# Optimization experiments

Measured on AMD Instinct MI355X. Metric: run time of the kernel, lower is better.

The kernel has to match this reference:

```python
import jax, jax.numpy as jnp
import numpy as np

B, S, R = 1, 128, 384          # batch, n_seq (MSA rows), n_res
C_M, C_Z, H, D = 256, 128, 8, 32  # msa channels, pair channels, heads, head dim


def layernorm(x, g, b, eps=1e-5):
    mu = jnp.mean(x, axis=-1, keepdims=True)
    var = jnp.var(x, axis=-1, keepdims=True)
    return (x - mu) * jax.lax.rsqrt(var + eps) * g + b


def setup_inputs() -> dict:
    key = jax.random.key(0)
    ks = jax.random.split(key, 10)
    w = lambda k, shape: jax.random.normal(k, shape, jnp.float32) * 0.02
    return {
        "msa_act": jax.random.normal(ks[0], (B, S, R, C_M), jnp.float32),
        "pair_act": jax.random.normal(ks[1], (B, R, R, C_Z), jnp.float32),
        "msa_mask": jnp.ones((B, S, R), jnp.float32),
        "qn_g": jnp.ones((C_M,), jnp.float32),
        "qn_b": jnp.zeros((C_M,), jnp.float32),
        "pn_g": jnp.ones((C_Z,), jnp.float32),
        "pn_b": jnp.zeros((C_Z,), jnp.float32),
        "w_pair": w(ks[2], (C_Z, H)),           # feat_2d_weights (no bias)
        "wq": w(ks[3], (C_M, H, D)),
        "wk": w(ks[4], (C_M, H, D)),
        "wv": w(ks[5], (C_M, H, D)),
        "wg": w(ks[6], (C_M, H, D)),            # gating linear
        "bg": jnp.ones((H, D), jnp.float32),     # gating bias (AF2 inits to 1)
        "wo": w(ks[7], (H, D, C_M)),             # output projection
        "bo": jnp.zeros((C_M,), jnp.float32),
    }


def reference(msa_act, pair_act, msa_mask, qn_g, qn_b, pn_g, pn_b,
              w_pair, wq, wk, wv, wg, bg, wo, bo):
    # pair bias: LN + Linear(c_z -> H), -> [B, 1, H, R, R]
    z = jnp.einsum('bijc,ch->bhij', layernorm(pair_act, pn_g, pn_b), w_pair)[:, None]
    # mask bias: [B, S, 1, 1, R]
    mask_bias = (1e9 * (msa_mask - 1.0))[:, :, None, None, :]

    m = layernorm(msa_act, qn_g, qn_b)
    q = jnp.einsum('bsrc,chd->bshrd', m, wq) * (D ** -0.5)
    k = jnp.einsum('bsrc,chd->bshrd', m, wk)
    v = jnp.einsum('bsrc,chd->bshrd', m, wv)

    logits = jnp.einsum('bshqd,bshkd->bshqk', q, k) + mask_bias + z  # [B,S,H,R,R]
    a = jax.nn.softmax(logits, axis=-1)
    o = jnp.einsum('bshqk,bshkd->bsqhd', a, v)                       # [B,S,R,H,D]

    g = jax.nn.sigmoid(jnp.einsum('bsrc,chd->bsrhd', m, wg) + bg)
    out = jnp.einsum('bsrhd,hdc->bsrc', o * g, wo) + bo              # [B,S,R,C_M]
    return out
```

## Files before the change

### kernel.cpp

```cpp
#include <hip/hip_runtime.h>
#include <hip/hip_bf16.h>

typedef unsigned int uint;
typedef unsigned short ushortT;
typedef __attribute__((ext_vector_type(8))) short bf16x8;
typedef __attribute__((ext_vector_type(4))) float f32x4;

#define S_ 128
#define R_ 384
#define CM 256
#define CZ 128
#define H_ 8
#define D_ 32
#define SR (S_*R_)
#define RRTOT (R_*R_)
#define SHRD (S_*H_*R_*D_)

__device__ __forceinline__ float bf2f(ushortT u) {
    return __uint_as_float(((uint)u) << 16);
}
__device__ __forceinline__ ushortT f2bf(float f) {
    uint x = __float_as_uint(f);
    x += 0x7FFFu + ((x >> 16) & 1u);
    return (ushortT)(x >> 16);
}
__device__ __forceinline__ uint pack_bf2(float lo, float hi) {
    return (uint)f2bf(lo) | ((uint)f2bf(hi) << 16);
}

__global__ __launch_bounds__(256) void k_prep(
        const float* __restrict__ wq, const float* __restrict__ wk,
        const float* __restrict__ wv, const float* __restrict__ wg,
        const float* __restrict__ wo,
        ushortT* __restrict__ wt, ushortT* __restrict__ wgt,
        ushortT* __restrict__ wot) {
    int id = blockIdx.x * 256 + threadIdx.x;
    int which = id >> 16, r16 = id & 65535;
    int y = r16 & 255, x = r16 >> 8;
    if (which == 0)      wt[(size_t)y*256 + x]       = f2bf(wq[(size_t)x*256 + y] * 0.17677669529663687f);
    else if (which == 1) wt[(size_t)(256+y)*256 + x] = f2bf(wk[(size_t)x*256 + y]);
    else if (which == 2) wt[(size_t)(512+y)*256 + x] = f2bf(wv[(size_t)x*256 + y]);
    else if (which == 3) wgt[(size_t)y*256 + x]      = f2bf(wg[(size_t)x*256 + y]);
    else                 wot[(size_t)y*256 + x]      = f2bf(wo[(size_t)x*256 + y]);
}

__global__ __launch_bounds__(256) void k_pair_bias(
        const float* __restrict__ pair, const float* __restrict__ pn_g,
        const float* __restrict__ pn_b, const float* __restrict__ w_pair,
        ushortT* __restrict__ z) {
    int wave = threadIdx.x >> 6, lane = threadIdx.x & 63;
    int row = blockIdx.x * 4 + wave;
    const float* x = pair + (size_t)row * CZ;
    float2 xv = *(const float2*)&x[lane * 2];
    float s  = xv.x + xv.y;
    float s2 = xv.x*xv.x + xv.y*xv.y;
    #pragma unroll
    for (int off = 32; off; off >>= 1) {
        s  += __shfl_xor(s,  off);
        s2 += __shfl_xor(s2, off);
    }
    float mu  = s * (1.0f / 128.0f);
    float var = s2 * (1.0f / 128.0f) - mu * mu;
    float rstd = rsqrtf(var + 1e-5f);
    float2 gv = *(const float2*)&pn_g[lane * 2];
    float2 bv = *(const float2*)&pn_b[lane * 2];
    float n0 = (xv.x - mu) * rstd * gv.x + bv.x;
    float n1 = (xv.y - mu) * rstd * gv.y + bv.y;
    float4 wa = *(const float4*)&w_pair[lane*16     ];
    float4 wb = *(const float4*)&w_pair[lane*16 +  4];
    float4 wc = *(const float4*)&w_pair[lane*16 +  8];
    float4 wd = *(const float4*)&w_pair[lane*16 + 12];
    float v0_ = n0*wa.x + n1*wc.x, v1_ = n0*wa.y + n1*wc.y;
    float v2_ = n0*wa.z + n1*wc.z, v3_ = n0*wa.w + n1*wc.w;
    float v4_ = n0*wb.x + n1*wd.x, v5_ = n0*wb.y + n1*wd.y;
    float v6_ = n0*wb.z + n1*wd.z, v7_ = n0*wb.w + n1*wd.w;
    float x0 = __shfl_xor(v0_,1), x1 = __shfl_xor(v1_,1), x2 = __shfl_xor(v2_,1), x3 = __shfl_xor(v3_,1);
    float x4 = __shfl_xor(v4_,1), x5 = __shfl_xor(v5_,1), x6 = __shfl_xor(v6_,1), x7 = __shfl_xor(v7_,1);
    bool b0 = (lane & 1) != 0;
    float u0 = b0 ? v4_+x4 : v0_+x0;
    float u1 = b0 ? v5_+x5 : v1_+x1;
    float u2 = b0 ? v6_+x6 : v2_+x2;
    float u3 = b0 ? v7_+x7 : v3_+x3;
    float y0 = __shfl_xor(u0,2), y1 = __shfl_xor(u1,2), y2 = __shfl_xor(u2,2), y3 = __shfl_xor(u3,2);
    bool b1 = (lane & 2) != 0;
    float w0 = b1 ? u2+y2 : u0+y0;
    float w1 = b1 ? u3+y3 : u1+y1;
    float z0 = __shfl_xor(w0,4), z1 = __shfl_xor(w1,4);
    bool b2 = (lane & 4) != 0;
    float val = b2 ? w1+z1 : w0+z0;
    val += __shfl_xor(val, 8);
    val += __shfl_xor(val, 16);
    val += __shfl_xor(val, 32);
    int hmap = 4*(lane & 1) + 2*((lane >> 1) & 1) + ((lane >> 2) & 1);
    if (lane < 8) z[(size_t)hmap * RRTOT + row] = f2bf(val);
}

__device__ __forceinline__ void ln_row_f4(
        const float* __restrict__ src, const float* __restrict__ gam,
        const float* __restrict__ bet, char* msb, int row, int lane) {
    float4 xv = *(const float4*)&src[lane * 4];
    float sm = (xv.x + xv.y) + (xv.z + xv.w);
    float s2 = (xv.x*xv.x + xv.y*xv.y) + (xv.z*xv.z + xv.w*xv.w);
    #pragma unroll
    for (int off = 32; off; off >>= 1) {
        sm += __shfl_xor(sm, off);
        s2 += __shfl_xor(s2, off);
    }
    float mu  = sm * (1.0f / 256.0f);
    float var = s2 * (1.0f / 256.0f) - mu * mu;
    float rstd = rsqrtf(var + 1e-5f);
    float4 gv = *(const float4*)&gam[lane * 4];
    float4 bv = *(const float4*)&bet[lane * 4];
    float n0 = (xv.x - mu) * rstd * gv.x + bv.x, n1 = (xv.y - mu) * rstd * gv.y + bv.y;
    float n2 = (xv.z - mu) * rstd * gv.z + bv.z, n3 = (xv.w - mu) * rstd * gv.w + bv.w;
    uint2 w; w.x = pack_bf2(n0, n1); w.y = pack_bf2(n2, n3);
    *(uint2*)(msb + ((row*512 + lane*8) ^ ((row & 7) << 4))) = w;
}

__global__ __launch_bounds__(256) void k_msa_qkv(
        const float* __restrict__ msa, const float* __restrict__ qn_g,
        const float* __restrict__ qn_b, const ushortT* __restrict__ wt,
        ushortT* __restrict__ qo, ushortT* __restrict__ ko,
        ushortT* __restrict__ vto) {
    __shared__ ushortT m_sh[32 * 256];
    __shared__ ushortT o_sh[32 * 256];
    int tid = threadIdx.x, wave = tid >> 6, lane = tid & 63;
    int c = lane & 15, g = (lane >> 4) & 3;
    int r0 = blockIdx.x * 32, s = r0 / R_, rl0 = r0 % R_;
    char* msb = (char*)m_sh;
    char* osb = (char*)o_sh;

    #pragma unroll
    for (int i = 0; i < 8; ++i) {
        int row = wave * 8 + i;
        ln_row_f4(msa + (size_t)(r0 + row) * CM, qn_g, qn_b, msb, row, lane);
    }
    __syncthreads();

    bf16x8 af[2][8];
    #pragma unroll
    for (int rt = 0; rt < 2; ++rt)
        #pragma unroll
        for (int kc = 0; kc < 8; ++kc) {
            int row = rt*16 + c;
            af[rt][kc] = *(const bf16x8*)(msb + ((row*512 + (kc*32 + 8*g)*2) ^ ((c & 7) << 4)));
        }

    const f32x4 z4 = {0.f, 0.f, 0.f, 0.f};
    for (int mI = 0; mI < 3; ++mI) {
        int tb = wave * 4;
        const ushortT* wb0 = wt + ((size_t)(mI*256 + tb*16 + c)) * 256 + 8*g;
        const ushortT* wb1 = wb0 + 16*256;
        const ushortT* wb2 = wb0 + 32*256;
        const ushortT* wb3 = wb0 + 48*256;
        f32x4 a0L = z4, a0H = z4, a1L = z4, a1H = z4;
        f32x4 a2L = z4, a2H = z4, a3L = z4, a3H = z4;
        #pragma unroll
        for (int kc = 0; kc < 8; ++kc) {
            bf16x8 b0 = *(const bf16x8*)(wb0 + kc*32);
            bf16x8 b1 = *(const bf16x8*)(wb1 + kc*32);
            bf16x8 b2 = *(const bf16x8*)(wb2 + kc*32);
            bf16x8 b3 = *(const bf16x8*)(wb3 + kc*32);
            a0L = __builtin_amdgcn_mfma_f32_16x16x32_bf16(af[0][kc], b0, a0L, 0, 0, 0);
            a0H = __builtin_amdgcn_mfma_f32_16x16x32_bf16(af[1][kc], b0, a0H, 0, 0, 0);
            a1L = __builtin_amdgcn_mfma_f32_16x16x32_bf16(af[0][kc], b1, a1L, 0, 0, 0);
            a1H = __builtin_amdgcn_mfma_f32_16x16x32_bf16(af[1][kc], b1, a1H, 0, 0, 0);
            a2L = __builtin_amdgcn_mfma_f32_16x16x32_bf16(af[0][kc], b2, a2L, 0, 0, 0);
            a2H = __builtin_amdgcn_mfma_f32_16x16x32_bf16(af[1][kc], b2, a2H, 0, 0, 0);
            a3L = __builtin_amdgcn_mfma_f32_16x16x32_bf16(af[0][kc], b3, a3L, 0, 0, 0);
            a3H = __builtin_amdgcn_mfma_f32_16x16x32_bf16(af[1][kc], b3, a3H, 0, 0, 0);
        }
        #pragma unroll
        for (int j = 0; j < 4; ++j) {
            f32x4 lo = (j == 0) ? a0L : (j == 1) ? a1L : (j == 2) ? a2L : a3L;
            f32x4 hi = (j == 0) ? a0H : (j == 1) ? a1H : (j == 2) ? a2H : a3H;
            if (mI < 2) {
                int col = (tb + j)*16 + c;
                #pragma unroll
                for (int r = 0; r < 4; ++r) {
                    int row0 = 4*g + r, row1 = row0 + 16;
                    *(ushortT*)(osb + ((row0*512 + col*2) ^ ((row0 & 7) << 4))) = f2bf(lo[r]);
                    *(ushortT*)(osb + ((row1*512 + col*2) ^ ((row1 & 7) << 4))) = f2bf(hi[r]);
                }
            } else {
                int hd = (tb + j)*16 + c;
                #pragma unroll
                for (int r = 0; r < 4; ++r) {
                    int rlo = 4*g + r, rhi = rlo + 16;
                    *(ushortT*)(osb + ((hd*64 + rlo*2) ^ ((hd & 3) << 4))) = f2bf(lo[r]);
                    *(ushortT*)(osb + ((hd*64 + rhi*2) ^ ((hd & 3) << 4))) = f2bf(hi[r]);
                }
            }
        }
        __syncthreads();
        if (mI < 2) {
            ushortT* O = (mI == 0) ? qo : ko;
            #pragma unroll
            for (int i = 0; i < 4; ++i) {
                int idx = tid + i*256;
                int row = idx >> 5, c16 = idx & 31;
                uint4 vd = *(const uint4*)(osb + ((row*512 + c16*16) ^ ((row & 7) << 4)));
                int hh = c16 >> 2, dq = (c16 & 3) * 8;
                size_t ga = ((size_t)(s*H_ + hh) * R_ + rl0 + row) * D_ + dq;
                *(uint4*)&O[ga] = vd;
            }
        } else {
            #pragma unroll
            for (int i = 0; i < 4; ++i) {
                int idx = tid + i*256;
                int hd = idx >> 2, q8 = idx & 3;
                uint4 vd = *(const uint4*)(osb + ((hd*64 + q8*16) ^ ((hd & 3) << 4)));
                size_t ga = ((size_t)(s*256 + hd)) * R_ + rl0 + q8*8;
                *(uint4*)&vto[ga] = vd;
            }
        }
        __syncthreads();
    }
}

__global__ __launch_bounds__(512) void k_attn(
        const ushortT* __restrict__ qws, const ushortT* __restrict__ kws,
        const ushortT* __restrict__ vtws, const ushortT* __restrict__ zws,
        const float* __restrict__ mask, float* __restrict__ out) {
    __shared__ ushortT k_sh[R_ * 40];
    __shared__ ushortT vt_sh[D_ * R_];
    __shared__ float   mb[R_];
    __shared__ ushortT p_sh[8 * 1280];
    int tid = threadIdx.x, wave = tid >> 6, lane = tid & 63;
    int c = lane & 15, g = (lane >> 4) & 3;
    int s = blockIdx.x >> 3, h = blockIdx.x & 7;
    size_t base = (size_t)(s * H_ + h) * R_ * D_;

    {
        const uint4* ks = (const uint4*)(kws + base);
        char* kb_ = (char*)k_sh;
        for (int i = tid; i < 1536; i += 512) {
            int row = i >> 2, part = i & 3;
            *(uint4*)(kb_ + row*80 + part*16) = ks[i];
        }
        const uint4* vs = (const uint4*)(vtws + base);
        char* vb = (char*)vt_sh;
        for (int i = tid; i < 1536; i += 512) {
            int d = i / 48, ch = i % 48;
            *(uint4*)(vb + ((d*768 + ch*16) ^ ((d & 7) << 4))) = vs[i];
        }
        for (int j = tid; j < R_; j += 512) mb[j] = 1e9f * (mask[s*R_ + j] - 1.0f);
    }
    __syncthreads();

    const char* ksb = (const char*)k_sh;
    const char* vtb = (const char*)vt_sh;
    char* psb = (char*)p_sh + wave * 2560;
    const f32x4 zero4 = {0.f, 0.f, 0.f, 0.f};

    for (int qt = wave; qt < 24; qt += 8) {
        int q0 = qt * 16;
        bf16x8 qf = *(const bf16x8*)(qws + base + (size_t)(q0 + c) * D_ + 8*g);
        const ushortT* zq = zws + (size_t)h * RRTOT + (size_t)(q0 + c) * R_ + 4*g;

        float sm = 0.f;
        f32x4 o0 = zero4, o1 = zero4;
        #pragma unroll 2
        for (int kb = 0; kb < 12; ++kb) {
            bf16x8 kfA = *(const bf16x8*)(ksb + ((2*kb    )*16 + c)*80 + 16*g);
            bf16x8 kfB = *(const bf16x8*)(ksb + ((2*kb + 1)*16 + c)*80 + 16*g);
            f32x4 pA = __builtin_amdgcn_mfma_f32_16x16x32_bf16(kfA, qf, zero4, 0, 0, 0);
            f32x4 pB = __builtin_amdgcn_mfma_f32_16x16x32_bf16(kfB, qf, zero4, 0, 0, 0);
            float4 mvA = *(const float4*)&mb[(2*kb    )*16 + 4*g];
            float4 mvB = *(const float4*)&mb[(2*kb + 1)*16 + 4*g];
            ushort4 zvA = *(const ushort4*)(zq + (2*kb    )*16);
            ushort4 zvB = *(const ushort4*)(zq + (2*kb + 1)*16);
            pA.x = __expf(pA.x + mvA.x + bf2f(zvA.x));
            pA.y = __expf(pA.y + mvA.y + bf2f(zvA.y));
            pA.z = __expf(pA.z + mvA.z + bf2f(zvA.z));
            pA.w = __expf(pA.w + mvA.w + bf2f(zvA.w));
            pB.x = __expf(pB.x + mvB.x + bf2f(zvB.x));
            pB.y = __expf(pB.y + mvB.y + bf2f(zvB.y));
            pB.z = __expf(pB.z + mvB.z + bf2f(zvB.z));
            pB.w = __expf(pB.w + mvB.w + bf2f(zvB.w));
            sm += (pA.x + pA.y) + (pA.z + pA.w) + (pB.x + pB.y) + (pB.z + pB.w);
            uint2 wA; wA.x = pack_bf2(pA.x, pA.y); wA.y = pack_bf2(pA.z, pA.w);
            uint2 wB; wB.x = pack_bf2(pB.x, pB.y); wB.y = pack_bf2(pB.z, pB.w);
            *(uint2*)(psb + (kb&1)*1280 + c*80 +      8*g) = wA;
            *(uint2*)(psb + (kb&1)*1280 + c*80 + 32 + 8*g) = wB;
            bf16x8 pa = *(const bf16x8*)(psb + (kb&1)*1280 + c*80 + 16*g);
            bf16x8 v0 = *(const bf16x8*)(vtb + (((c     )*768 + kb*64 + 16*g) ^ ((c & 7) << 4)));
            bf16x8 v1 = *(const bf16x8*)(vtb + (((16 + c)*768 + kb*64 + 16*g) ^ ((c & 7) << 4)));
            o0 = __builtin_amdgcn_mfma_f32_16x16x32_bf16(v0, pa, o0, 0, 0, 0);
            o1 = __builtin_amdgcn_mfma_f32_16x16x32_bf16(v1, pa, o1, 0, 0, 0);
        }
        sm += __shfl_xor(sm, 16);
        sm += __shfl_xor(sm, 32);
        float inv = 1.0f / sm;
        float4 s0, s1;
        s0.x = o0[0]*inv; s0.y = o0[1]*inv; s0.z = o0[2]*inv; s0.w = o0[3]*inv;
        s1.x = o1[0]*inv; s1.y = o1[1]*inv; s1.z = o1[2]*inv; s1.w = o1[3]*inv;
        float* ob = out + (size_t)(s*R_ + q0 + c) * CM + h*D_ + 4*g;
        *(float4*)ob = s0;
        *(float4*)(ob + 16) = s1;
    }
}

__global__ __launch_bounds__(256) void k_out(
        const float* __restrict__ msa, const float* __restrict__ qn_g,
        const float* __restrict__ qn_b, const ushortT* __restrict__ wgt,
        const float* __restrict__ bg, const ushortT* __restrict__ wot,
        const float* __restrict__ bo, float* __restrict__ out) {
    __shared__ ushortT m_sh[32 * 256];
    __shared__ ushortT og_sh[32 * 256];
    int tid = threadIdx.x, wave = tid >> 6, lane = tid & 63;
    int c = lane & 15, g = (lane >> 4) & 3;
    int r0 = blockIdx.x * 32;
    char* msb = (char*)m_sh;
    char* ogb = (char*)og_sh;

    #pragma unroll
    for (int i = 0; i < 8; ++i) {
        int row = wave * 8 + i;
        ln_row_f4(msa + (size_t)(r0 + row) * CM, qn_g, qn_b, msb, row, lane);
    }
    __syncthreads();

    bf16x8 af[2][8];
    #pragma unroll
    for (int rt = 0; rt < 2; ++rt)
        #pragma unroll
        for (int kc = 0; kc < 8; ++kc) {
            int row = rt*16 + c;
            af[rt][kc] = *(const bf16x8*)(msb + ((row*512 + (kc*32 + 8*g)*2) ^ ((c & 7) << 4)));
        }

    const f32x4 z4 = {0.f, 0.f, 0.f, 0.f};
    {
        int tb = wave * 4;
        const ushortT* wb0 = wgt + (size_t)(tb*16 + c) * 256 + 8*g;
        const ushortT* wb1 = wb0 + 16*256;
        const ushortT* wb2 = wb0 + 32*256;
        const ushortT* wb3 = wb0 + 48*256;
        f32x4 a0L = z4, a0H = z4, a1L = z4, a1H = z4;
        f32x4 a2L = z4, a2H = z4, a3L = z4, a3H = z4;
        #pragma unroll
        for (int kc = 0; kc < 8; ++kc) {
            bf16x8 b0 = *(const bf16x8*)(wb0 + kc*32);
            bf16x8 b1 = *(const bf16x8*)(wb1 + kc*32);
            bf16x8 b2 = *(const bf16x8*)(wb2 + kc*32);
            bf16x8 b3 = *(const bf16x8*)(wb3 + kc*32);
            a0L = __builtin_amdgcn_mfma_f32_16x16x32_bf16(af[0][kc], b0, a0L, 0, 0, 0);
            a0H = __builtin_amdgcn_mfma_f32_16x16x32_bf16(af[1][kc], b0, a0H, 0, 0, 0);
            a1L = __builtin_amdgcn_mfma_f32_16x16x32_bf16(af[0][kc], b1, a1L, 0, 0, 0);
            a1H = __builtin_amdgcn_mfma_f32_16x16x32_bf16(af[1][kc], b1, a1H, 0, 0, 0);
            a2L = __builtin_amdgcn_mfma_f32_16x16x32_bf16(af[0][kc], b2, a2L, 0, 0, 0);
            a2H = __builtin_amdgcn_mfma_f32_16x16x32_bf16(af[1][kc], b2, a2H, 0, 0, 0);
            a3L = __builtin_amdgcn_mfma_f32_16x16x32_bf16(af[0][kc], b3, a3L, 0, 0, 0);
            a3H = __builtin_amdgcn_mfma_f32_16x16x32_bf16(af[1][kc], b3, a3H, 0, 0, 0);
        }
        #pragma unroll
        for (int j = 0; j < 4; ++j) {
            f32x4 lo = (j == 0) ? a0L : (j == 1) ? a1L : (j == 2) ? a2L : a3L;
            f32x4 hi = (j == 0) ? a0H : (j == 1) ? a1H : (j == 2) ? a2H : a3H;
            int t = (tb + j)*16 + c;
            float bgv = bg[t];
            #pragma unroll
            for (int r = 0; r < 4; ++r) {
                int row0 = 4*g + r, row1 = row0 + 16;
                float g0 = 1.0f / (1.0f + __expf(-(lo[r] + bgv)));
                float g1 = 1.0f / (1.0f + __expf(-(hi[r] + bgv)));
                float ov0 = out[(size_t)(r0 + row0) * CM + t];
                float ov1 = out[(size_t)(r0 + row1) * CM + t];
                *(ushortT*)(ogb + ((row0*512 + t*2) ^ ((row0 & 7) << 4))) = f2bf(ov0 * g0);
                *(ushortT*)(ogb + ((row1*512 + t*2) ^ ((row1 & 7) << 4))) = f2bf(ov1 * g1);
            }
        }
    }
    __syncthreads();

    bf16x8 af2[2][8];
    #pragma unroll
    for (int rt = 0; rt < 2; ++rt)
        #pragma unroll
        for (int kc = 0; kc < 8; ++kc) {
            int row = rt*16 + c;
            af2[rt][kc] = *(const bf16x8*)(ogb + ((row*512 + (kc*32 + 8*g)*2) ^ ((c & 7) << 4)));
        }

    {
        int tb = wave * 4;
        const ushortT* wb0 = wot + (size_t)(tb*16 + c) * 256 + 8*g;
        const ushortT* wb1 = wb0 + 16*256;
        const ushortT* wb2 = wb0 + 32*256;
        const ushortT* wb3 = wb0 + 48*256;
        f32x4 a0L = z4, a0H = z4, a1L = z4, a1H = z4;
        f32x4 a2L = z4, a2H = z4, a3L = z4, a3H = z4;
        #pragma unroll
        for (int kc = 0; kc < 8; ++kc) {
            bf16x8 b0 = *(const bf16x8*)(wb0 + kc*32);
            bf16x8 b1 = *(const bf16x8*)(wb1 + kc*32);
            bf16x8 b2 = *(const bf16x8*)(wb2 + kc*32);
            bf16x8 b3 = *(const bf16x8*)(wb3 + kc*32);
            a0L = __builtin_amdgcn_mfma_f32_16x16x32_bf16(af2[0][kc], b0, a0L, 0, 0, 0);
            a0H = __builtin_amdgcn_mfma_f32_16x16x32_bf16(af2[1][kc], b0, a0H, 0, 0, 0);
            a1L = __builtin_amdgcn_mfma_f32_16x16x32_bf16(af2[0][kc], b1, a1L, 0, 0, 0);
            a1H = __builtin_amdgcn_mfma_f32_16x16x32_bf16(af2[1][kc], b1, a1H, 0, 0, 0);
            a2L = __builtin_amdgcn_mfma_f32_16x16x32_bf16(af2[0][kc], b2, a2L, 0, 0, 0);
            a2H = __builtin_amdgcn_mfma_f32_16x16x32_bf16(af2[1][kc], b2, a2H, 0, 0, 0);
            a3L = __builtin_amdgcn_mfma_f32_16x16x32_bf16(af2[0][kc], b3, a3L, 0, 0, 0);
            a3H = __builtin_amdgcn_mfma_f32_16x16x32_bf16(af2[1][kc], b3, a3H, 0, 0, 0);
        }
        #pragma unroll
        for (int j = 0; j < 4; ++j) {
            f32x4 lo = (j == 0) ? a0L : (j == 1) ? a1L : (j == 2) ? a2L : a3L;
            f32x4 hi = (j == 0) ? a0H : (j == 1) ? a1H : (j == 2) ? a2H : a3H;
            int t = (tb + j)*16 + c;
            float bov = bo[t];
            #pragma unroll
            for (int r = 0; r < 4; ++r) {
                int row0 = 4*g + r, row1 = row0 + 16;
                out[(size_t)(r0 + row0) * CM + t] = lo[r] + bov;
                out[(size_t)(r0 + row1) * CM + t] = hi[r] + bov;
            }
        }
    }
}

extern "C" void kernel_launch(void* const* d_in, const int* in_sizes, int n_in,
                              void* d_out, int out_size, void* d_ws, size_t ws_size,
                              hipStream_t stream) {
    const float* msa    = (const float*)d_in[0];
    const float* pair   = (const float*)d_in[1];
    const float* mask   = (const float*)d_in[2];
    const float* qn_g   = (const float*)d_in[3];
    const float* qn_b   = (const float*)d_in[4];
    const float* pn_g   = (const float*)d_in[5];
    const float* pn_b   = (const float*)d_in[6];
    const float* w_pair = (const float*)d_in[7];
    const float* wq     = (const float*)d_in[8];
    const float* wk     = (const float*)d_in[9];
    const float* wv     = (const float*)d_in[10];
    const float* wg     = (const float*)d_in[11];
    const float* bg     = (const float*)d_in[12];
    const float* wo     = (const float*)d_in[13];
    const float* bo     = (const float*)d_in[14];
    float* out = (float*)d_out;

    ushortT* qws  = (ushortT*)d_ws;
    ushortT* kws  = qws + (size_t)SHRD;
    ushortT* vtws = kws + (size_t)SHRD;
    ushortT* zws  = vtws + (size_t)SHRD;
    ushortT* wt   = zws + (size_t)H_ * RRTOT;
    ushortT* wgt  = wt + 3 * 65536;
    ushortT* wot  = wgt + 65536;

    k_prep     <<<1280,    256, 0, stream>>>(wq, wk, wv, wg, wo, wt, wgt, wot);
    k_pair_bias<<<RRTOT/4, 256, 0, stream>>>(pair, pn_g, pn_b, w_pair, zws);
    k_msa_qkv  <<<SR/32,   256, 0, stream>>>(msa, qn_g, qn_b, wt, qws, kws, vtws);
    k_attn     <<<S_*H_,   512, 0, stream>>>(qws, kws, vtws, zws, mask, out);
    k_out      <<<SR/32,   256, 0, stream>>>(msa, qn_g, qn_b, wgt, bg, wot, bo, out);
}
```

Before: 287.4 us.

## Fuse QKV projection into attention kernel and share a precomputed LayerNorm buffer

Result: no change. 291.8 us (+1.5%).

```diff
diff --git a/kernel.cpp b/kernel.cpp
--- a/kernel.cpp
+++ b/kernel.cpp
@@ -14,7 +14,6 @@
 #define D_ 32
 #define SR (S_*R_)
 #define RRTOT (R_*R_)
-#define SHRD (S_*H_*R_*D_)
 
 __device__ __forceinline__ float bf2f(ushortT u) {
     return __uint_as_float(((uint)u) << 16);
@@ -95,10 +94,7 @@
     if (lane < 8) z[(size_t)hmap * RRTOT + row] = f2bf(val);
 }
 
-__device__ __forceinline__ void ln_row_f4(
-        const float* __restrict__ src, const float* __restrict__ gam,
-        const float* __restrict__ bet, char* msb, int row, int lane) {
-    float4 xv = *(const float4*)&src[lane * 4];
+__device__ __forceinline__ uint2 ln_reduce(float4 xv, float4 gv, float4 bv) {
     float sm = (xv.x + xv.y) + (xv.z + xv.w);
     float s2 = (xv.x*xv.x + xv.y*xv.y) + (xv.z*xv.z + xv.w*xv.w);
     #pragma unroll
@@ -109,119 +105,43 @@
     float mu  = sm * (1.0f / 256.0f);
     float var = s2 * (1.0f / 256.0f) - mu * mu;
     float rstd = rsqrtf(var + 1e-5f);
-    float4 gv = *(const float4*)&gam[lane * 4];
-    float4 bv = *(const float4*)&bet[lane * 4];
-    float n0 = (xv.x - mu) * rstd * gv.x + bv.x, n1 = (xv.y - mu) * rstd * gv.y + bv.y;
-    float n2 = (xv.z - mu) * rstd * gv.z + bv.z, n3 = (xv.w - mu) * rstd * gv.w + bv.w;
-    uint2 w; w.x = pack_bf2(n0, n1); w.y = pack_bf2(n2, n3);
-    *(uint2*)(msb + ((row*512 + lane*8) ^ ((row & 7) << 4))) = w;
-}
-
-__global__ __launch_bounds__(256) void k_msa_qkv(
+    uint2 w;
+    w.x = pack_bf2((xv.x - mu)*rstd*gv.x + bv.x, (xv.y - mu)*rstd*gv.y + bv.y);
+    w.y = pack_bf2((xv.z - mu)*rstd*gv.z + bv.z, (xv.w - mu)*rstd*gv.w + bv.w);
+    return w;
+}
+
+__global__ __launch_bounds__(256) void k_ln(
         const float* __restrict__ msa, const float* __restrict__ qn_g,
-        const float* __restrict__ qn_b, const ushortT* __restrict__ wt,
-        ushortT* __restrict__ qo, ushortT* __restrict__ ko,
-        ushortT* __restrict__ vto) {
-    __shared__ ushortT m_sh[32 * 256];
-    __shared__ ushortT o_sh[32 * 256];
-    int tid = threadIdx.x, wave = tid >> 6, lane = tid & 63;
-    int c = lane & 15, g = (lane >> 4) & 3;
-    int r0 = blockIdx.x * 32, s = r0 / R_, rl0 = r0 % R_;
-    char* msb = (char*)m_sh;
-    char* osb = (char*)o_sh;
-
-    #pragma unroll
-    for (int i = 0; i < 8; ++i) {
-        int row = wave * 8 + i;
-        ln_row_f4(msa + (size_t)(r0 + row) * CM, qn_g, qn_b, msb, row, lane);
-    }
-    __syncthreads();
-
-    bf16x8 af[2][8];
-    #pragma unroll
-    for (int rt = 0; rt < 2; ++rt)
-        #pragma unroll
-        for (int kc = 0; kc < 8; ++kc) {
-            int row = rt*16 + c;
-            af[rt][kc] = *(const bf16x8*)(msb + ((row*512 + (kc*32 + 8*g)*2) ^ ((c & 7) << 4)));
-        }
-
-    const f32x4 z4 = {0.f, 0.f, 0.f, 0.f};
-    for (int mI = 0; mI < 3; ++mI) {
-        int tb = wave * 4;
-        const ushortT* wb0 = wt + ((size_t)(mI*256 + tb*16 + c)) * 256 + 8*g;
-        const ushortT* wb1 = wb0 + 16*256;
-        const ushortT* wb2 = wb0 + 32*256;
-        const ushortT* wb3 = wb0 + 48*256;
-        f32x4 a0L = z4, a0H = z4, a1L = z4, a1H = z4;
-        f32x4 a2L = z4, a2H = z4, a3L = z4, a3H = z4;
-        #pragma unroll
-        for (int kc = 0; kc < 8; ++kc) {
-            bf16x8 b0 = *(const bf16x8*)(wb0 + kc*32);
-            bf16x8 b1 = *(const bf16x8*)(wb1 + kc*32);
-            bf16x8 b2 = *(const bf16x8*)(wb2 + kc*32);
-            bf16x8 b3 = *(const bf16x8*)(wb3 + kc*32);
-            a0L = __builtin_amdgcn_mfma_f32_16x16x32_bf16(af[0][kc], b0, a0L, 0, 0, 0);
-            a0H = __builtin_amdgcn_mfma_f32_16x16x32_bf16(af[1][kc], b0, a0H, 0, 0, 0);
-            a1L = __builtin_amdgcn_mfma_f32_16x16x32_bf16(af[0][kc], b1, a1L, 0, 0, 0);
-            a1H = __builtin_amdgcn_mfma_f32_16x16x32_bf16(af[1][kc], b1, a1H, 0, 0, 0);
-            a2L = __builtin_amdgcn_mfma_f32_16x16x32_bf16(af[0][kc], b2, a2L, 0, 0, 0);
-            a2H = __builtin_amdgcn_mfma_f32_16x16x32_bf16(af[1][kc], b2, a2H, 0, 0, 0);
-            a3L = __builtin_amdgcn_mfma_f32_16x16x32_bf16(af[0][kc], b3, a3L, 0, 0, 0);
-            a3H = __builtin_amdgcn_mfma_f32_16x16x32_bf16(af[1][kc], b3, a3H, 0, 0, 0);
-        }
-        #pragma unroll
-        for (int j = 0; j < 4; ++j) {
-            f32x4 lo = (j == 0) ? a0L : (j == 1) ? a1L : (j == 2) ? a2L : a3L;
-            f32x4 hi = (j == 0) ? a0H : (j == 1) ? a1H : (j == 2) ? a2H : a3H;
-            if (mI < 2) {
-                int col = (tb + j)*16 + c;
-                #pragma unroll
-                for (int r = 0; r < 4; ++r) {
-                    int row0 = 4*g + r, row1 = row0 + 16;
-                    *(ushortT*)(osb + ((row0*512 + col*2) ^ ((row0 & 7) << 4))) = f2bf(lo[r]);
-                    *(ushortT*)(osb + ((row1*512 + col*2) ^ ((row1 & 7) << 4))) = f2bf(hi[r]);
-                }
-            } else {
-                int hd = (tb + j)*16 + c;
-                #pragma unroll
-                for (int r = 0; r < 4; ++r) {
-                    int rlo = 4*g + r, rhi = rlo + 16;
-                    *(ushortT*)(osb + ((hd*64 + rlo*2) ^ ((hd & 3) << 4))) = f2bf(lo[r]);
-                    *(ushortT*)(osb + ((hd*64 + rhi*2) ^ ((hd & 3) << 4))) = f2bf(hi[r]);
-                }
-            }
-        }
-        __syncthreads();
-        if (mI < 2) {
-            ushortT* O = (mI == 0) ? qo : ko;
-            #pragma unroll
-            for (int i = 0; i < 4; ++i) {
-                int idx = tid + i*256;
-                int row = idx >> 5, c16 = idx & 31;
-                uint4 vd = *(const uint4*)(osb + ((row*512 + c16*16) ^ ((row & 7) << 4)));
-                int hh = c16 >> 2, dq = (c16 & 3) * 8;
-                size_t ga = ((size_t)(s*H_ + hh) * R_ + rl0 + row) * D_ + dq;
-                *(uint4*)&O[ga] = vd;
-            }
-        } else {
-            #pragma unroll
-            for (int i = 0; i < 4; ++i) {
-                int idx = tid + i*256;
-                int hd = idx >> 2, q8 = idx & 3;
-                uint4 vd = *(const uint4*)(osb + ((hd*64 + q8*16) ^ ((hd & 3) << 4)));
-                size_t ga = ((size_t)(s*256 + hd)) * R_ + rl0 + q8*8;
-                *(uint4*)&vto[ga] = vd;
-            }
-        }
-        __syncthreads();
-    }
-}
-
-__global__ __launch_bounds__(512) void k_attn(
-        const ushortT* __restrict__ qws, const ushortT* __restrict__ kws,
-        const ushortT* __restrict__ vtws, const ushortT* __restrict__ zws,
-        const float* __restrict__ mask, float* __restrict__ out) {
+        const float* __restrict__ qn_b, ushortT* __restrict__ m) {
+    int wave = threadIdx.x >> 6, lane = threadIdx.x & 63;
+    int r0 = blockIdx.x * 32 + wave * 8;
+    const float* src = msa + (size_t)r0 * CM + lane * 4;
+    float4 x0 = *(const float4*)(src        );
+    float4 x1 = *(const float4*)(src + 1*CM );
+    float4 x2 = *(const float4*)(src + 2*CM );
+    float4 x3 = *(const float4*)(src + 3*CM );
+    float4 x4 = *(const float4*)(src + 4*CM );
+    float4 x5 = *(const float4*)(src + 5*CM );
+    float4 x6 = *(const float4*)(src + 6*CM );
+    float4 x7 = *(const float4*)(src + 7*CM );
+    float4 gv = *(const float4*)&qn_g[lane*4];
+    float4 bv = *(const float4*)&qn_b[lane*4];
+    ushortT* dst = m + (size_t)r0 * CM + lane * 4;
+    *(uint2*)(dst       ) = ln_reduce(x0, gv, bv);
+    *(uint2*)(dst + 1*CM) = ln_reduce(x1, gv, bv);
+    *(uint2*)(dst + 2*CM) = ln_reduce(x2, gv, bv);
+    *(uint2*)(dst + 3*CM) = ln_reduce(x3, gv, bv);
+    *(uint2*)(dst + 4*CM) = ln_reduce(x4, gv, bv);
+    *(uint2*)(dst + 5*CM) = ln_reduce(x5, gv, bv);
+    *(uint2*)(dst + 6*CM) = ln_reduce(x6, gv, bv);
+    *(uint2*)(dst + 7*CM) = ln_reduce(x7, gv, bv);
+}
+
+__global__ __launch_bounds__(512) void k_attn_f(
+        const ushortT* __restrict__ m, const ushortT* __restrict__ wt,
+        const ushortT* __restrict__ zws, const float* __restrict__ mask,
+        float* __restrict__ out) {
     __shared__ ushortT k_sh[R_ * 40];
     __shared__ ushortT vt_sh[D_ * R_];
     __shared__ float   mb[R_];
@@ -229,33 +149,70 @@
     int tid = threadIdx.x, wave = tid >> 6, lane = tid & 63;
     int c = lane & 15, g = (lane >> 4) & 3;
     int s = blockIdx.x >> 3, h = blockIdx.x & 7;
-    size_t base = (size_t)(s * H_ + h) * R_ * D_;
-
-    {
-        const uint4* ks = (const uint4*)(kws + base);
-        char* kb_ = (char*)k_sh;
-        for (int i = tid; i < 1536; i += 512) {
-            int row = i >> 2, part = i & 3;
-            *(uint4*)(kb_ + row*80 + part*16) = ks[i];
-        }
-        const uint4* vs = (const uint4*)(vtws + base);
-        char* vb = (char*)vt_sh;
-        for (int i = tid; i < 1536; i += 512) {
-            int d = i / 48, ch = i % 48;
-            *(uint4*)(vb + ((d*768 + ch*16) ^ ((d & 7) << 4))) = vs[i];
-        }
-        for (int j = tid; j < R_; j += 512) mb[j] = 1e9f * (mask[s*R_ + j] - 1.0f);
+    const ushortT* mrow = m + (size_t)s * R_ * CM;
+    char* kb_ = (char*)k_sh;
+    char* vb_ = (char*)vt_sh;
+    char* psb = (char*)p_sh + wave * 2560;
+    const f32x4 zero4 = {0.f, 0.f, 0.f, 0.f};
+
+    for (int j = tid; j < R_; j += 512) mb[j] = 1e9f * (mask[s*R_ + j] - 1.0f);
+
+    const ushortT* wkb = wt + ((size_t)(256 + 2*h*16 + c)) * 256 + 8*g;
+    const ushortT* wvb = wt + ((size_t)(512 + 2*h*16 + c)) * 256 + 8*g;
+    #pragma unroll 1
+    for (int rt = 0; rt < 3; ++rt) {
+        int rbase = wave * 48 + rt * 16;
+        bf16x8 afr[8];
+        #pragma unroll
+        for (int kc = 0; kc < 8; ++kc)
+            afr[kc] = *(const bf16x8*)(mrow + (size_t)(rbase + c) * CM + kc*32 + 8*g);
+        f32x4 ka0 = zero4, ka1 = zero4, va0 = zero4, va1 = zero4;
+        #pragma unroll
+        for (int kc = 0; kc < 8; ++kc) {
+            bf16x8 bk0 = *(const bf16x8*)(wkb + kc*32);
+            bf16x8 bk1 = *(const bf16x8*)(wkb + 16*256 + kc*32);
+            bf16x8 bv0 = *(const bf16x8*)(wvb + kc*32);
+            bf16x8 bv1 = *(const bf16x8*)(wvb + 16*256 + kc*32);
+            ka0 = __builtin_amdgcn_mfma_f32_16x16x32_bf16(afr[kc], bk0, ka0, 0, 0, 0);
+            ka1 = __builtin_amdgcn_mfma_f32_16x16x32_bf16(afr[kc], bk1, ka1, 0, 0, 0);
+            va0 = __builtin_amdgcn_mfma_f32_16x16x32_bf16(afr[kc], bv0, va0, 0, 0, 0);
+            va1 = __builtin_amdgcn_mfma_f32_16x16x32_bf16(afr[kc], bv1, va1, 0, 0, 0);
+        }
+        #pragma unroll
+        for (int r = 0; r < 4; ++r) {
+            int krow = rbase + 4*g + r;
+            *(ushortT*)(kb_ + krow*80 + c*2)        = f2bf(ka0[r]);
+            *(ushortT*)(kb_ + krow*80 + (16+c)*2)   = f2bf(ka1[r]);
+            *(ushortT*)(vb_ + ((c*768      + krow*2) ^ ((c & 7) << 4))) = f2bf(va0[r]);
+            *(ushortT*)(vb_ + (((16+c)*768 + krow*2) ^ ((c & 7) << 4))) = f2bf(va1[r]);
+        }
     }
     __syncthreads();
 
     const char* ksb = (const char*)k_sh;
     const char* vtb = (const char*)vt_sh;
-    char* psb = (char*)p_sh + wave * 2560;
-    const f32x4 zero4 = {0.f, 0.f, 0.f, 0.f};
 
     for (int qt = wave; qt < 24; qt += 8) {
         int q0 = qt * 16;
-        bf16x8 qf = *(const bf16x8*)(qws + base + (size_t)(q0 + c) * D_ + 8*g);
+        bf16x8 afq[8];
+        #pragma unroll
+        for (int kc = 0; kc < 8; ++kc)
+            afq[kc] = *(const bf16x8*)(mrow + (size_t)(q0 + c) * CM + kc*32 + 8*g);
+        f32x4 qa0 = zero4, qa1 = zero4;
+        const ushortT* wqb = wt + ((size_t)(2*h*16 + c)) * 256 + 8*g;
+        #pragma unroll
+        for (int kc = 0; kc < 8; ++kc) {
+            bf16x8 bq0 = *(const bf16x8*)(wqb + kc*32);
+            bf16x8 bq1 = *(const bf16x8*)(wqb + 16*256 + kc*32);
+            qa0 = __builtin_amdgcn_mfma_f32_16x16x32_bf16(afq[kc], bq0, qa0, 0, 0, 0);
+            qa1 = __builtin_amdgcn_mfma_f32_16x16x32_bf16(afq[kc], bq1, qa1, 0, 0, 0);
+        }
+        #pragma unroll
+        for (int r = 0; r < 4; ++r) {
+            *(ushortT*)(psb + (4*g + r)*80 + c*2)      = f2bf(qa0[r]);
+            *(ushortT*)(psb + (4*g + r)*80 + (16+c)*2) = f2bf(qa1[r]);
+        }
+        bf16x8 qf = *(const bf16x8*)(psb + c*80 + 16*g);
         const ushortT* zq = zws + (size_t)h * RRTOT + (size_t)(q0 + c) * R_ + 4*g;
 
         float sm = 0.f;
@@ -301,59 +258,49 @@
     }
 }
 
-__global__ __launch_bounds__(256) void k_out(
-        const float* __restrict__ msa, const float* __restrict__ qn_g,
-        const float* __restrict__ qn_b, const ushortT* __restrict__ wgt,
+#define MFMA_GROUP4(AF, WB)                                                          \
+    {                                                                                \
+        _Pragma("unroll")                                                            \
+        for (int kc = 0; kc < 8; ++kc) {                                             \
+            bf16x8 b0 = *(const bf16x8*)((WB) + kc*32);                              \
+            bf16x8 b1 = *(const bf16x8*)((WB) + 16*256 + kc*32);                     \
+            bf16x8 b2 = *(const bf16x8*)((WB) + 32*256 + kc*32);                     \
+            bf16x8 b3 = *(const bf16x8*)((WB) + 48*256 + kc*32);                     \
+            a0L = __builtin_amdgcn_mfma_f32_16x16x32_bf16(AF[0][kc], b0, a0L, 0,0,0);\
+            a0H = __builtin_amdgcn_mfma_f32_16x16x32_bf16(AF[1][kc], b0, a0H, 0,0,0);\
+            a1L = __builtin_amdgcn_mfma_f32_16x16x32_bf16(AF[0][kc], b1, a1L, 0,0,0);\
+            a1H = __builtin_amdgcn_mfma_f32_16x16x32_bf16(AF[1][kc], b1, a1H, 0,0,0);\
+            a2L = __builtin_amdgcn_mfma_f32_16x16x32_bf16(AF[0][kc], b2, a2L, 0,0,0);\
+            a2H = __builtin_amdgcn_mfma_f32_16x16x32_bf16(AF[1][kc], b2, a2H, 0,0,0);\
+            a3L = __builtin_amdgcn_mfma_f32_16x16x32_bf16(AF[0][kc], b3, a3L, 0,0,0);\
+            a3H = __builtin_amdgcn_mfma_f32_16x16x32_bf16(AF[1][kc], b3, a3H, 0,0,0);\
+        }                                                                            \
+    }
+
+__global__ __launch_bounds__(256) void k_out_m(
+        const ushortT* __restrict__ m, const ushortT* __restrict__ wgt,
         const float* __restrict__ bg, const ushortT* __restrict__ wot,
         const float* __restrict__ bo, float* __restrict__ out) {
-    __shared__ ushortT m_sh[32 * 256];
     __shared__ ushortT og_sh[32 * 256];
     int tid = threadIdx.x, wave = tid >> 6, lane = tid & 63;
     int c = lane & 15, g = (lane >> 4) & 3;
     int r0 = blockIdx.x * 32;
-    char* msb = (char*)m_sh;
     char* ogb = (char*)og_sh;
-
-    #pragma unroll
-    for (int i = 0; i < 8; ++i) {
-        int row = wave * 8 + i;
-        ln_row_f4(msa + (size_t)(r0 + row) * CM, qn_g, qn_b, msb, row, lane);
-    }
-    __syncthreads();
 
     bf16x8 af[2][8];
     #pragma unroll
     for (int rt = 0; rt < 2; ++rt)
         #pragma unroll
-        for (int kc = 0; kc < 8; ++kc) {
-            int row = rt*16 + c;
-            af[rt][kc] = *(const bf16x8*)(msb + ((row*512 + (kc*32 + 8*g)*2) ^ ((c & 7) << 4)));
-        }
+        for (int kc = 0; kc < 8; ++kc)
+            af[rt][kc] = *(const bf16x8*)(m + (size_t)(r0 + rt*16 + c) * CM + kc*32 + 8*g);
 
     const f32x4 z4 = {0.f, 0.f, 0.f, 0.f};
     {
         int tb = wave * 4;
         const ushortT* wb0 = wgt + (size_t)(tb*16 + c) * 256 + 8*g;
-        const ushortT* wb1 = wb0 + 16*256;
-        const ushortT* wb2 = wb0 + 32*256;
-        const ushortT* wb3 = wb0 + 48*256;
         f32x4 a0L = z4, a0H = z4, a1L = z4, a1H = z4;
         f32x4 a2L = z4, a2H = z4, a3L = z4, a3H = z4;
-        #pragma unroll
-        for (int kc = 0; kc < 8; ++kc) {
-            bf16x8 b0 = *(const bf16x8*)(wb0 + kc*32);
-            bf16x8 b1 = *(const bf16x8*)(wb1 + kc*32);
-            bf16x8 b2 = *(const bf16x8*)(wb2 + kc*32);
-            bf16x8 b3 = *(const bf16x8*)(wb3 + kc*32);
-            a0L = __builtin_amdgcn_mfma_f32_16x16x32_bf16(af[0][kc], b0, a0L, 0, 0, 0);
-            a0H = __builtin_amdgcn_mfma_f32_16x16x32_bf16(af[1][kc], b0, a0H, 0, 0, 0);
-            a1L = __builtin_amdgcn_mfma_f32_16x16x32_bf16(af[0][kc], b1, a1L, 0, 0, 0);
-            a1H = __builtin_amdgcn_mfma_f32_16x16x32_bf16(af[1][kc], b1, a1H, 0, 0, 0);
-            a2L = __builtin_amdgcn_mfma_f32_16x16x32_bf16(af[0][kc], b2, a2L, 0, 0, 0);
-            a2H = __builtin_amdgcn_mfma_f32_16x16x32_bf16(af[1][kc], b2, a2H, 0, 0, 0);
-            a3L = __builtin_amdgcn_mfma_f32_16x16x32_bf16(af[0][kc], b3, a3L, 0, 0, 0);
-            a3H = __builtin_amdgcn_mfma_f32_16x16x32_bf16(af[1][kc], b3, a3H, 0, 0, 0);
-        }
+        MFMA_GROUP4(af, wb0);
         #pragma unroll
         for (int j = 0; j < 4; ++j) {
             f32x4 lo = (j == 0) ? a0L : (j == 1) ? a1L : (j == 2) ? a2L : a3L;
@@ -386,26 +333,9 @@
     {
         int tb = wave * 4;
         const ushortT* wb0 = wot + (size_t)(tb*16 + c) * 256 + 8*g;
-        const ushortT* wb1 = wb0 + 16*256;
-        const ushortT* wb2 = wb0 + 32*256;
-        const ushortT* wb3 = wb0 + 48*256;
         f32x4 a0L = z4, a0H = z4, a1L = z4, a1H = z4;
         f32x4 a2L = z4, a2H = z4, a3L = z4, a3H = z4;
-        #pragma unroll
-        for (int kc = 0; kc < 8; ++kc) {
-            bf16x8 b0 = *(const bf16x8*)(wb0 + kc*32);
-            bf16x8 b1 = *(const bf16x8*)(wb1 + kc*32);
-            bf16x8 b2 = *(const bf16x8*)(wb2 + kc*32);
-            bf16x8 b3 = *(const bf16x8*)(wb3 + kc*32);
-            a0L = __builtin_amdgcn_mfma_f32_16x16x32_bf16(af2[0][kc], b0, a0L, 0, 0, 0);
-            a0H = __builtin_amdgcn_mfma_f32_16x16x32_bf16(af2[1][kc], b0, a0H, 0, 0, 0);
-            a1L = __builtin_amdgcn_mfma_f32_16x16x32_bf16(af2[0][kc], b1, a1L, 0, 0, 0);
-            a1H = __builtin_amdgcn_mfma_f32_16x16x32_bf16(af2[1][kc], b1, a1H, 0, 0, 0);
-            a2L = __builtin_amdgcn_mfma_f32_16x16x32_bf16(af2[0][kc], b2, a2L, 0, 0, 0);
-            a2H = __builtin_amdgcn_mfma_f32_16x16x32_bf16(af2[1][kc], b2, a2H, 0, 0, 0);
-            a3L = __builtin_amdgcn_mfma_f32_16x16x32_bf16(af2[0][kc], b3, a3L, 0, 0, 0);
-            a3H = __builtin_amdgcn_mfma_f32_16x16x32_bf16(af2[1][kc], b3, a3H, 0, 0, 0);
-        }
+        MFMA_GROUP4(af2, wb0);
         #pragma unroll
         for (int j = 0; j < 4; ++j) {
             f32x4 lo = (j == 0) ? a0L : (j == 1) ? a1L : (j == 2) ? a2L : a3L;
@@ -442,17 +372,15 @@
     const float* bo     = (const float*)d_in[14];
     float* out = (float*)d_out;
 
-    ushortT* qws  = (ushortT*)d_ws;
-    ushortT* kws  = qws + (size_t)SHRD;
-    ushortT* vtws = kws + (size_t)SHRD;
-    ushortT* zws  = vtws + (size_t)SHRD;
-    ushortT* wt   = zws + (size_t)H_ * RRTOT;
-    ushortT* wgt  = wt + 3 * 65536;
-    ushortT* wot  = wgt + 65536;
+    ushortT* zws = (ushortT*)d_ws;
+    ushortT* wt  = zws + (size_t)H_ * RRTOT;
+    ushortT* wgt = wt + 3 * 65536;
+    ushortT* wot = wgt + 65536;
+    ushortT* mws = wot + 65536;
 
     k_prep     <<<1280,    256, 0, stream>>>(wq, wk, wv, wg, wo, wt, wgt, wot);
     k_pair_bias<<<RRTOT/4, 256, 0, stream>>>(pair, pn_g, pn_b, w_pair, zws);
-    k_msa_qkv  <<<SR/32,   256, 0, stream>>>(msa, qn_g, qn_b, wt, qws, kws, vtws);
-    k_attn     <<<S_*H_,   512, 0, stream>>>(qws, kws, vtws, zws, mask, out);
-    k_out      <<<SR/32,   256, 0, stream>>>(msa, qn_g, qn_b, wgt, bg, wot, bo, out);
-}
+    k_ln       <<<SR/32,   256, 0, stream>>>(msa, qn_g, qn_b, mws);
+    k_attn_f   <<<S_*H_,   512, 0, stream>>>(mws, wt, zws, mask, out);
+    k_out_m    <<<SR/32,   256, 0, stream>>>(mws, wgt, bg, wot, bo, out);
+}
```
